# Performance work log

Measured on AMD Instinct MI355X. Metric: run time of the kernel, lower is better.

The kernel has to match this reference:

```python
import jax, jax.numpy as jnp
import numpy as np

B = 2048
LATENT = 32
FRAME = 256
COND = 1
HIDDEN = 256
FUT = 1
E = 8
GATE_H = 64
IN_SIZE = LATENT + FRAME * COND      # 288
INTER = LATENT + HIDDEN              # 288 (must equal IN_SIZE, see forward)
OUT_SIZE = FUT * FRAME               # 256


def setup_inputs() -> dict:
    key = jax.random.key(0)
    ks = jax.random.split(key, 16)

    def kaiming(k, shape, fan_in):
        bound = np.sqrt(6.0 / fan_in).astype(np.float32)
        return jax.random.uniform(k, shape, jnp.float32, -bound, bound)

    z = jax.random.normal(ks[0], (B, IN_SIZE), jnp.float32)
    # gate MLP: Linear(IN_SIZE,64) -> ELU -> Linear(64,64) -> ELU -> Linear(64,E)
    g0_w = kaiming(ks[1], (IN_SIZE, GATE_H), IN_SIZE)
    g0_b = jnp.zeros((GATE_H,), jnp.float32)
    g1_w = kaiming(ks[2], (GATE_H, GATE_H), GATE_H)
    g1_b = jnp.zeros((GATE_H,), jnp.float32)
    g2_w = kaiming(ks[3], (GATE_H, E), GATE_H)
    g2_b = jnp.zeros((E,), jnp.float32)
    # expert layers (kaiming_uniform over [E, in, out]; bias filled with 0.01)
    w0 = kaiming(ks[4], (E, IN_SIZE, HIDDEN), IN_SIZE)
    b0 = jnp.full((E, HIDDEN), 0.01, jnp.float32)
    w1 = kaiming(ks[5], (E, INTER, HIDDEN), INTER)
    b1 = jnp.full((E, HIDDEN), 0.01, jnp.float32)
    w2 = kaiming(ks[6], (E, INTER, OUT_SIZE), INTER)
    b2 = jnp.full((E, OUT_SIZE), 0.01, jnp.float32)
    return dict(z=z, g0_w=g0_w, g0_b=g0_b, g1_w=g1_w, g1_b=g1_b,
                g2_w=g2_w, g2_b=g2_b, w0=w0, b0=b0, w1=w1, b1=b1, w2=w2, b2=b2)


def reference(z, g0_w, g0_b, g1_w, g1_b, g2_w, g2_b, w0, b0, w1, b1, w2, b2):
    # gating network -> softmax coefficients [B, E]
    h = jax.nn.elu(z @ g0_w + g0_b)
    h = jax.nn.elu(h @ g1_w + g1_b)
    coefficients = jax.nn.softmax(h @ g2_w + g2_b, axis=1)

    layers = [(w0, b0, True), (w1, b1, True), (w2, b2, False)]
    layer_out = None
    for weight, bias, has_act in layers:
        # materialize per-sample mixed weights (matches torch.matmul(coef, flat_weight).view(...))
        mixed_weight = jnp.einsum('be,eio->bio', coefficients, weight)  # [B, in, out]
        mixed_bias = coefficients @ bias                                 # [B, out]
        # baddbmm with z as [B,1,in]: per-sample vec-mat product
        out = jnp.einsum('bi,bio->bo', z, mixed_weight) + mixed_bias
        layer_out = jax.nn.elu(out) if has_act else out
    return layer_out
```

## Files before the change

kernel.cpp:

```cpp
#include <hip/hip_runtime.h>
#include <hip/hip_bf16.h>

#define B_TOTAL 2048
#define IN_SZ   288
#define GH      64
#define E_NUM   8
#define OUT_N   256
#define NKT     9

#define W2F_BLKS 72
#define ZF_BLKS  32
#define GWF_FRAGS 46

typedef __attribute__((ext_vector_type(8))) short bf16x8;
typedef __attribute__((ext_vector_type(4))) float f32x4;

__device__ __forceinline__ float elu_f(float x) {
    return x > 0.0f ? x : (expf(x) - 1.0f);
}
__device__ __forceinline__ ushort f2bf(float f) {
    __hip_bfloat16 h = __float2bfloat16(f);
    return *reinterpret_cast<ushort*>(&h);
}

__global__ __launch_bounds__(256) void prep_kernel(
    const float* __restrict__ w2, const float* __restrict__ z,
    const float* __restrict__ g0_w, const float* __restrict__ g1_w,
    const float* __restrict__ g2_w,
    ushort* __restrict__ w2f, ushort* __restrict__ zf, ushort* __restrict__ gwf)
{
    __shared__ float ts[32][260];
    const int t = threadIdx.x;
    const int wid = t >> 6, l = t & 63;
    const int fr = l & 15, fg = l >> 4;

    if (blockIdx.x < W2F_BLKS) {
        const int e  = blockIdx.x / NKT;
        const int kt = blockIdx.x - e * NKT;
        const float* src = w2 + ((size_t)e * IN_SZ + kt * 32) * OUT_N;
        #pragma unroll
        for (int q = t; q < 2048; q += 256) {
            int r = q >> 6, c4 = q & 63;
            *(float4*)&ts[r][c4 * 4] = *(const float4*)(src + (size_t)r * OUT_N + c4 * 4);
        }
        __syncthreads();
        #pragma unroll
        for (int it = 0; it < 4; ++it) {
            int q = t + it * 256;
            int nt = q >> 6, ll = q & 63;
            int qfr = ll & 15, qfg = ll >> 4;
            ushort4 u0, u1;
            u0.x = f2bf(ts[qfg * 8 + 0][nt * 16 + qfr]);
            u0.y = f2bf(ts[qfg * 8 + 1][nt * 16 + qfr]);
            u0.z = f2bf(ts[qfg * 8 + 2][nt * 16 + qfr]);
            u0.w = f2bf(ts[qfg * 8 + 3][nt * 16 + qfr]);
            u1.x = f2bf(ts[qfg * 8 + 4][nt * 16 + qfr]);
            u1.y = f2bf(ts[qfg * 8 + 5][nt * 16 + qfr]);
            u1.z = f2bf(ts[qfg * 8 + 6][nt * 16 + qfr]);
            u1.w = f2bf(ts[qfg * 8 + 7][nt * 16 + qfr]);
            size_t off = ((size_t)((e * 16 + nt) * NKT + kt)) * 512 + ll * 8;
            *(ushort4*)&w2f[off]     = u0;
            *(ushort4*)&w2f[off + 4] = u1;
        }
        return;
    }

    if (blockIdx.x < W2F_BLKS + ZF_BLKS) {
        const int mt = (blockIdx.x - W2F_BLKS) * 4 + wid;
        const int m0 = mt * 16;
        const float* zr = z + (size_t)(m0 + fr) * IN_SZ + fg * 8;
        #pragma unroll
        for (int kt = 0; kt < NKT; ++kt) {
            float4 v0 = *(const float4*)(zr + kt * 32);
            float4 v1 = *(const float4*)(zr + kt * 32 + 4);
            ushort4 u0, u1;
            u0.x = f2bf(v0.x); u0.y = f2bf(v0.y); u0.z = f2bf(v0.z); u0.w = f2bf(v0.w);
            u1.x = f2bf(v1.x); u1.y = f2bf(v1.y); u1.z = f2bf(v1.z); u1.w = f2bf(v1.w);
            size_t off = ((size_t)(mt * NKT + kt)) * 512 + l * 8;
            *(ushort4*)&zf[off]     = u0;
            *(ushort4*)&zf[off + 4] = u1;
        }
        return;
    }

    for (int fid = wid; fid < GWF_FRAGS; fid += 4) {
        float vals[8];
        if (fid < 36) {
            int nt = fid / NKT, kt = fid - nt * NKT;
            #pragma unroll
            for (int j = 0; j < 8; ++j) {
                int k = kt * 32 + fg * 8 + j;
                vals[j] = g0_w[k * GH + nt * 16 + fr];
            }
        } else if (fid < 44) {
            int q = fid - 36, nt = q >> 1, kk = q & 1;
            #pragma unroll
            for (int j = 0; j < 8; ++j) {
                int k = kk * 32 + fg * 8 + j;
                vals[j] = g1_w[k * GH + nt * 16 + fr];
            }
        } else {
            int kk = fid - 44;
            #pragma unroll
            for (int j = 0; j < 8; ++j) {
                int k = kk * 32 + fg * 8 + j;
                vals[j] = (fr < E_NUM) ? g2_w[k * E_NUM + fr] : 0.0f;
            }
        }
        ushort4 u0, u1;
        u0.x = f2bf(vals[0]); u0.y = f2bf(vals[1]); u0.z = f2bf(vals[2]); u0.w = f2bf(vals[3]);
        u1.x = f2bf(vals[4]); u1.y = f2bf(vals[5]); u1.z = f2bf(vals[6]); u1.w = f2bf(vals[7]);
        size_t off = (size_t)fid * 512 + l * 8;
        *(ushort4*)&gwf[off]     = u0;
        *(ushort4*)&gwf[off + 4] = u1;
    }
}

__global__ __launch_bounds__(256) void gate_kernel(
    const ushort* __restrict__ zf, const ushort* __restrict__ gwf,
    const float* __restrict__ g0_b, const float* __restrict__ g1_b,
    const float* __restrict__ g2_b,
    float* __restrict__ coefT)
{
    __shared__ ushort hscr_all[4][16][72];
    __shared__ float  lgs[64][8];

    const int t = threadIdx.x, wid = t >> 6, l = t & 63;
    const int fr = l & 15, fg = l >> 4, fk = fg * 8;
    const int r0 = blockIdx.x * 64;
    const int mt = blockIdx.x * 4 + wid;
    ushort (*hscr)[72] = hscr_all[wid];

    bf16x8 A[9];
    #pragma unroll
    for (int kt = 0; kt < NKT; ++kt)
        A[kt] = *(const bf16x8*)(zf + ((size_t)(mt * NKT + kt)) * 512 + l * 8);

    #pragma unroll
    for (int nt = 0; nt < 4; ++nt) {
        f32x4 g = {0.f, 0.f, 0.f, 0.f};
        #pragma unroll
        for (int kt = 0; kt < NKT; ++kt) {
            bf16x8 b = *(const bf16x8*)(gwf + ((size_t)(nt * NKT + kt)) * 512 + l * 8);
            g = __builtin_amdgcn_mfma_f32_16x16x32_bf16(A[kt], b, g, 0, 0, 0);
        }
        float bias = g0_b[nt * 16 + fr];
        #pragma unroll
        for (int j = 0; j < 4; ++j)
            hscr[fg * 4 + j][nt * 16 + fr] = f2bf(elu_f(g[j] + bias));
    }

    {
        bf16x8 hA[2];
        #pragma unroll
        for (int kk = 0; kk < 2; ++kk)
            hA[kk] = *(const bf16x8*)&hscr[fr][kk * 32 + fk];
        #pragma unroll
        for (int nt = 0; nt < 4; ++nt) {
            f32x4 g = {0.f, 0.f, 0.f, 0.f};
            #pragma unroll
            for (int kk = 0; kk < 2; ++kk) {
                bf16x8 b = *(const bf16x8*)(gwf + ((size_t)(36 + nt * 2 + kk)) * 512 + l * 8);
                g = __builtin_amdgcn_mfma_f32_16x16x32_bf16(hA[kk], b, g, 0, 0, 0);
            }
            float bias = g1_b[nt * 16 + fr];
            #pragma unroll
            for (int j = 0; j < 4; ++j)
                hscr[fg * 4 + j][nt * 16 + fr] = f2bf(elu_f(g[j] + bias));
        }
    }

    {
        bf16x8 hA[2];
        #pragma unroll
        for (int kk = 0; kk < 2; ++kk)
            hA[kk] = *(const bf16x8*)&hscr[fr][kk * 32 + fk];
        f32x4 g = {0.f, 0.f, 0.f, 0.f};
        #pragma unroll
        for (int kk = 0; kk < 2; ++kk) {
            bf16x8 b = *(const bf16x8*)(gwf + ((size_t)(44 + kk)) * 512 + l * 8);
            g = __builtin_amdgcn_mfma_f32_16x16x32_bf16(hA[kk], b, g, 0, 0, 0);
        }
        if (fr < E_NUM) {
            float bias = g2_b[fr];
            #pragma unroll
            for (int j = 0; j < 4; ++j)
                lgs[wid * 16 + fg * 4 + j][fr] = g[j] + bias;
        }
    }
    __syncthreads();

    if (t < 64) {
        float m = lgs[t][0];
        #pragma unroll
        for (int k = 1; k < E_NUM; ++k) m = fmaxf(m, lgs[t][k]);
        float s = 0.f;
        float ex[E_NUM];
        #pragma unroll
        for (int k = 0; k < E_NUM; ++k) { ex[k] = expf(lgs[t][k] - m); s += ex[k]; }
        float inv = 1.0f / s;
        #pragma unroll
        for (int k = 0; k < E_NUM; ++k)
            coefT[(size_t)k * B_TOTAL + r0 + t] = ex[k] * inv;
    }
}

__global__ __launch_bounds__(64) void gemm_kernel(
    const ushort* __restrict__ zf, const ushort* __restrict__ w2f,
    const float* __restrict__ coefT, const float* __restrict__ b2,
    float* __restrict__ out)
{
    const int l = threadIdx.x, fr = l & 15, fg = l >> 4;
    const int mt = blockIdx.x, m0 = mt * 16;
    const int nt = blockIdx.y, n0 = nt * 16;

    bf16x8 A[9];
    #pragma unroll
    for (int kt = 0; kt < NKT; ++kt)
        A[kt] = *(const bf16x8*)(zf + ((size_t)(mt * NKT + kt)) * 512 + l * 8);

    const ushort* Bp = w2f + (size_t)nt * NKT * 512 + l * 8;

    f32x4 acc = {0.f, 0.f, 0.f, 0.f};
    bf16x8 B[9];
    #pragma unroll
    for (int kt = 0; kt < NKT; ++kt)
        B[kt] = *(const bf16x8*)(Bp + (size_t)kt * 512);

    #pragma unroll
    for (int e = 0; e < E_NUM; ++e) {
        bf16x8 Bn[9];
        if (e < E_NUM - 1) {
            #pragma unroll
            for (int kt = 0; kt < NKT; ++kt)
                Bn[kt] = *(const bf16x8*)(Bp + ((size_t)(e + 1) * 16 * NKT + kt) * 512);
        }
        f32x4 p0 = {0.f, 0.f, 0.f, 0.f};
        f32x4 p1 = {0.f, 0.f, 0.f, 0.f};
        p0 = __builtin_amdgcn_mfma_f32_16x16x32_bf16(A[0], B[0], p0, 0, 0, 0);
        p1 = __builtin_amdgcn_mfma_f32_16x16x32_bf16(A[1], B[1], p1, 0, 0, 0);
        p0 = __builtin_amdgcn_mfma_f32_16x16x32_bf16(A[2], B[2], p0, 0, 0, 0);
        p1 = __builtin_amdgcn_mfma_f32_16x16x32_bf16(A[3], B[3], p1, 0, 0, 0);
        p0 = __builtin_amdgcn_mfma_f32_16x16x32_bf16(A[4], B[4], p0, 0, 0, 0);
        p1 = __builtin_amdgcn_mfma_f32_16x16x32_bf16(A[5], B[5], p1, 0, 0, 0);
        p0 = __builtin_amdgcn_mfma_f32_16x16x32_bf16(A[6], B[6], p0, 0, 0, 0);
        p1 = __builtin_amdgcn_mfma_f32_16x16x32_bf16(A[7], B[7], p1, 0, 0, 0);
        p0 = __builtin_amdgcn_mfma_f32_16x16x32_bf16(A[8], B[8], p0, 0, 0, 0);

        float4 cv = *(const float4*)(coefT + (size_t)e * B_TOTAL + m0 + fg * 4);
        float bv  = b2[e * OUT_N + n0 + fr];
        float ca[4] = {cv.x, cv.y, cv.z, cv.w};
        #pragma unroll
        for (int j = 0; j < 4; ++j)
            acc[j] = fmaf(ca[j], p0[j] + p1[j] + bv, acc[j]);

        #pragma unroll
        for (int kt = 0; kt < NKT; ++kt) B[kt] = Bn[kt];
    }

    #pragma unroll
    for (int j = 0; j < 4; ++j)
        out[(size_t)(m0 + fg * 4 + j) * OUT_N + n0 + fr] = acc[j];
}

__global__ __launch_bounds__(64) void gate_fb_kernel(
    const float* __restrict__ z,
    const float* __restrict__ g0_w, const float* __restrict__ g0_b,
    const float* __restrict__ g1_w, const float* __restrict__ g1_b,
    const float* __restrict__ g2_w, const float* __restrict__ g2_b,
    float* __restrict__ coef)
{
    __shared__ float z_s[IN_SZ];
    __shared__ float h0_s[GH];
    __shared__ float h1_s[GH];
    const int b = blockIdx.x;
    const int t = threadIdx.x;
    const float* zr = z + (size_t)b * IN_SZ;
    for (int i = t; i < IN_SZ; i += 64) z_s[i] = zr[i];
    __syncthreads();
    float a0 = g0_b[t];
    for (int i = 0; i < IN_SZ; ++i) a0 = fmaf(z_s[i], g0_w[i * GH + t], a0);
    h0_s[t] = elu_f(a0);
    __syncthreads();
    float a1 = g1_b[t];
    for (int k = 0; k < GH; ++k) a1 = fmaf(h0_s[k], g1_w[k * GH + t], a1);
    h1_s[t] = elu_f(a1);
    __syncthreads();
    if (t < E_NUM) {
        float lg = g2_b[t];
        for (int k = 0; k < GH; ++k) lg = fmaf(h1_s[k], g2_w[k * E_NUM + t], lg);
        float m = lg;
        for (int d = 1; d < 8; d <<= 1) m = fmaxf(m, __shfl_xor(m, d, 8));
        float ex = expf(lg - m);
        float s = ex;
        for (int d = 1; d < 8; d <<= 1) s += __shfl_xor(s, d, 8);
        coef[b * E_NUM + t] = ex / s;
    }
}

__global__ __launch_bounds__(256) void direct_kernel(
    const float* __restrict__ z, const float* __restrict__ w2,
    const float* __restrict__ b2, const float* __restrict__ coef,
    float* __restrict__ out)
{
    __shared__ float z_s[8][IN_SZ];
    __shared__ float c_s[8][E_NUM];
    const int b0 = blockIdx.x * 8;
    const int t  = threadIdx.x;
    for (int idx = t; idx < 8 * IN_SZ; idx += 256)
        ((float*)z_s)[idx] = z[(size_t)b0 * IN_SZ + idx];
    if (t < 64) c_s[t >> 3][t & 7] = coef[b0 * E_NUM + t];
    __syncthreads();
    float outv[8];
    #pragma unroll
    for (int r = 0; r < 8; ++r) outv[r] = 0.0f;
    for (int e = 0; e < E_NUM; ++e) {
        const float* w = w2 + (size_t)e * IN_SZ * OUT_N + t;
        float tmp[8];
        #pragma unroll
        for (int r = 0; r < 8; ++r) tmp[r] = 0.0f;
        #pragma unroll 4
        for (int i = 0; i < IN_SZ; ++i) {
            float wv = w[i * OUT_N];
            #pragma unroll
            for (int r = 0; r < 8; ++r) tmp[r] += z_s[r][i] * wv;
        }
        float bv = b2[e * OUT_N + t];
        #pragma unroll
        for (int r = 0; r < 8; ++r) outv[r] += c_s[r][e] * (tmp[r] + bv);
    }
    #pragma unroll
    for (int r = 0; r < 8; ++r) out[(size_t)(b0 + r) * OUT_N + t] = outv[r];
}

extern "C" void kernel_launch(void* const* d_in, const int* in_sizes, int n_in,
                              void* d_out, int out_size, void* d_ws, size_t ws_size,
                              hipStream_t stream) {
    const float* z    = (const float*)d_in[0];
    const float* g0_w = (const float*)d_in[1];
    const float* g0_b = (const float*)d_in[2];
    const float* g1_w = (const float*)d_in[3];
    const float* g1_b = (const float*)d_in[4];
    const float* g2_w = (const float*)d_in[5];
    const float* g2_b = (const float*)d_in[6];
    const float* w2   = (const float*)d_in[11];
    const float* b2   = (const float*)d_in[12];
    float* out = (float*)d_out;

    const size_t w2f_b   = (size_t)E_NUM * 16 * NKT * 1024;
    const size_t zf_b    = (size_t)128 * NKT * 1024;
    const size_t gwf_b   = (size_t)GWF_FRAGS * 1024;
    const size_t coefT_b = (size_t)E_NUM * B_TOTAL * sizeof(float);

    char* p = (char*)d_ws;
    ushort* w2f   = (ushort*)p;            p += w2f_b;
    ushort* zf    = (ushort*)p;            p += zf_b;
    ushort* gwf   = (ushort*)p;            p += gwf_b;
    float*  coefT = (float*)p;

    if (ws_size >= w2f_b + zf_b + gwf_b + coefT_b) {
        prep_kernel<<<W2F_BLKS + ZF_BLKS + 1, 256, 0, stream>>>(
            w2, z, g0_w, g1_w, g2_w, w2f, zf, gwf);
        gate_kernel<<<32, 256, 0, stream>>>(zf, gwf, g0_b, g1_b, g2_b, coefT);
        gemm_kernel<<<dim3(B_TOTAL / 16, OUT_N / 16), 64, 0, stream>>>(
            zf, w2f, coefT, b2, out);
    } else {
        float* coef = (float*)d_ws;
        gate_fb_kernel<<<B_TOTAL, 64, 0, stream>>>(z, g0_w, g0_b, g1_w, g1_b,
                                                   g2_w, g2_b, coef);
        direct_kernel<<<B_TOTAL / 8, 256, 0, stream>>>(z, w2, b2, coef, out);
    }
}
```

Measured before the change: 24.20 us.

## Fuse gate network into prep kernel and tile GEMM over two row tiles

The gating MLP is folded into the prep kernel: the z-conversion blocks now also run the gate, reading gate weights straight from fp32 and converting them to bf16 in registers instead of going through a separate gate kernel and a pre-packed weight buffer. This removes one kernel launch and the gwf round trip, at the cost of redundant gate-weight loads and conversions in every block, plus extra block-wide barriers. The GEMM kernel now computes two 16-row tiles per block, reusing each loaded expert weight fragment for both tiles and halving the grid, which raises register pressure.

```diff
diff --git a/kernel.cpp b/kernel.cpp
--- a/kernel.cpp
+++ b/kernel.cpp
@@ -9,8 +9,7 @@
 #define NKT     9
 
 #define W2F_BLKS 72
-#define ZF_BLKS  32
-#define GWF_FRAGS 46
+#define ZG_BLKS  32
 
 typedef __attribute__((ext_vector_type(8))) short bf16x8;
 typedef __attribute__((ext_vector_type(4))) float f32x4;
@@ -25,16 +24,18 @@
 
 __global__ __launch_bounds__(256) void prep_kernel(
     const float* __restrict__ w2, const float* __restrict__ z,
-    const float* __restrict__ g0_w, const float* __restrict__ g1_w,
-    const float* __restrict__ g2_w,
-    ushort* __restrict__ w2f, ushort* __restrict__ zf, ushort* __restrict__ gwf)
+    const float* __restrict__ g0_w, const float* __restrict__ g0_b,
+    const float* __restrict__ g1_w, const float* __restrict__ g1_b,
+    const float* __restrict__ g2_w, const float* __restrict__ g2_b,
+    ushort* __restrict__ w2f, ushort* __restrict__ zf, float* __restrict__ coefT)
 {
-    __shared__ float ts[32][260];
+    __shared__ char smem[33536];
     const int t = threadIdx.x;
     const int wid = t >> 6, l = t & 63;
     const int fr = l & 15, fg = l >> 4;
 
     if (blockIdx.x < W2F_BLKS) {
+        float (*ts)[260] = (float(*)[260])smem;
         const int e  = blockIdx.x / NKT;
         const int kt = blockIdx.x - e * NKT;
         const float* src = w2 + ((size_t)e * IN_SZ + kt * 32) * OUT_N;
@@ -65,83 +66,39 @@
         return;
     }
 
-    if (blockIdx.x < W2F_BLKS + ZF_BLKS) {
-        const int mt = (blockIdx.x - W2F_BLKS) * 4 + wid;
-        const int m0 = mt * 16;
-        const float* zr = z + (size_t)(m0 + fr) * IN_SZ + fg * 8;
-        #pragma unroll
-        for (int kt = 0; kt < NKT; ++kt) {
-            float4 v0 = *(const float4*)(zr + kt * 32);
-            float4 v1 = *(const float4*)(zr + kt * 32 + 4);
-            ushort4 u0, u1;
-            u0.x = f2bf(v0.x); u0.y = f2bf(v0.y); u0.z = f2bf(v0.z); u0.w = f2bf(v0.w);
-            u1.x = f2bf(v1.x); u1.y = f2bf(v1.y); u1.z = f2bf(v1.z); u1.w = f2bf(v1.w);
-            size_t off = ((size_t)(mt * NKT + kt)) * 512 + l * 8;
-            *(ushort4*)&zf[off]     = u0;
-            *(ushort4*)&zf[off + 4] = u1;
-        }
-        return;
-    }
-
-    for (int fid = wid; fid < GWF_FRAGS; fid += 4) {
-        float vals[8];
-        if (fid < 36) {
-            int nt = fid / NKT, kt = fid - nt * NKT;
-            #pragma unroll
-            for (int j = 0; j < 8; ++j) {
-                int k = kt * 32 + fg * 8 + j;
-                vals[j] = g0_w[k * GH + nt * 16 + fr];
-            }
-        } else if (fid < 44) {
-            int q = fid - 36, nt = q >> 1, kk = q & 1;
-            #pragma unroll
-            for (int j = 0; j < 8; ++j) {
-                int k = kk * 32 + fg * 8 + j;
-                vals[j] = g1_w[k * GH + nt * 16 + fr];
-            }
-        } else {
-            int kk = fid - 44;
-            #pragma unroll
-            for (int j = 0; j < 8; ++j) {
-                int k = kk * 32 + fg * 8 + j;
-                vals[j] = (fr < E_NUM) ? g2_w[k * E_NUM + fr] : 0.0f;
-            }
-        }
-        ushort4 u0, u1;
-        u0.x = f2bf(vals[0]); u0.y = f2bf(vals[1]); u0.z = f2bf(vals[2]); u0.w = f2bf(vals[3]);
-        u1.x = f2bf(vals[4]); u1.y = f2bf(vals[5]); u1.z = f2bf(vals[6]); u1.w = f2bf(vals[7]);
-        size_t off = (size_t)fid * 512 + l * 8;
-        *(ushort4*)&gwf[off]     = u0;
-        *(ushort4*)&gwf[off + 4] = u1;
-    }
-}
-
-__global__ __launch_bounds__(256) void gate_kernel(
-    const ushort* __restrict__ zf, const ushort* __restrict__ gwf,
-    const float* __restrict__ g0_b, const float* __restrict__ g1_b,
-    const float* __restrict__ g2_b,
-    float* __restrict__ coefT)
-{
-    __shared__ ushort hscr_all[4][16][72];
-    __shared__ float  lgs[64][8];
-
-    const int t = threadIdx.x, wid = t >> 6, l = t & 63;
-    const int fr = l & 15, fg = l >> 4, fk = fg * 8;
-    const int r0 = blockIdx.x * 64;
-    const int mt = blockIdx.x * 4 + wid;
-    ushort (*hscr)[72] = hscr_all[wid];
+    ushort (*hscr)[72] = (ushort(*)[72])(smem + wid * 2304);
+    float  (*lgs)[8]   = (float(*)[8])(smem + 4 * 2304 + wid * 512);
+
+    const int mt = (blockIdx.x - W2F_BLKS) * 4 + wid;
+    const int m0 = mt * 16;
 
     bf16x8 A[9];
-    #pragma unroll
-    for (int kt = 0; kt < NKT; ++kt)
-        A[kt] = *(const bf16x8*)(zf + ((size_t)(mt * NKT + kt)) * 512 + l * 8);
+    const float* zr = z + (size_t)(m0 + fr) * IN_SZ + fg * 8;
+    #pragma unroll
+    for (int kt = 0; kt < NKT; ++kt) {
+        float4 v0 = *(const float4*)(zr + kt * 32);
+        float4 v1 = *(const float4*)(zr + kt * 32 + 4);
+        bf16x8 a;
+        a[0] = (short)f2bf(v0.x); a[1] = (short)f2bf(v0.y);
+        a[2] = (short)f2bf(v0.z); a[3] = (short)f2bf(v0.w);
+        a[4] = (short)f2bf(v1.x); a[5] = (short)f2bf(v1.y);
+        a[6] = (short)f2bf(v1.z); a[7] = (short)f2bf(v1.w);
+        A[kt] = a;
+        *(bf16x8*)(zf + ((size_t)(mt * NKT + kt)) * 512 + l * 8) = a;
+    }
 
     #pragma unroll
     for (int nt = 0; nt < 4; ++nt) {
         f32x4 g = {0.f, 0.f, 0.f, 0.f};
         #pragma unroll
         for (int kt = 0; kt < NKT; ++kt) {
-            bf16x8 b = *(const bf16x8*)(gwf + ((size_t)(nt * NKT + kt)) * 512 + l * 8);
+            float vals[8];
+            #pragma unroll
+            for (int j = 0; j < 8; ++j)
+                vals[j] = g0_w[(kt * 32 + fg * 8 + j) * GH + nt * 16 + fr];
+            bf16x8 b;
+            #pragma unroll
+            for (int j = 0; j < 8; ++j) b[j] = (short)f2bf(vals[j]);
             g = __builtin_amdgcn_mfma_f32_16x16x32_bf16(A[kt], b, g, 0, 0, 0);
         }
         float bias = g0_b[nt * 16 + fr];
@@ -149,59 +106,79 @@
         for (int j = 0; j < 4; ++j)
             hscr[fg * 4 + j][nt * 16 + fr] = f2bf(elu_f(g[j] + bias));
     }
+    __syncthreads();
 
     {
         bf16x8 hA[2];
         #pragma unroll
         for (int kk = 0; kk < 2; ++kk)
-            hA[kk] = *(const bf16x8*)&hscr[fr][kk * 32 + fk];
+            hA[kk] = *(const bf16x8*)&hscr[fr][kk * 32 + fg * 8];
+        f32x4 gacc[4];
         #pragma unroll
         for (int nt = 0; nt < 4; ++nt) {
             f32x4 g = {0.f, 0.f, 0.f, 0.f};
             #pragma unroll
             for (int kk = 0; kk < 2; ++kk) {
-                bf16x8 b = *(const bf16x8*)(gwf + ((size_t)(36 + nt * 2 + kk)) * 512 + l * 8);
+                float vals[8];
+                #pragma unroll
+                for (int j = 0; j < 8; ++j)
+                    vals[j] = g1_w[(kk * 32 + fg * 8 + j) * GH + nt * 16 + fr];
+                bf16x8 b;
+                #pragma unroll
+                for (int j = 0; j < 8; ++j) b[j] = (short)f2bf(vals[j]);
                 g = __builtin_amdgcn_mfma_f32_16x16x32_bf16(hA[kk], b, g, 0, 0, 0);
             }
+            gacc[nt] = g;
+        }
+        __syncthreads();
+        #pragma unroll
+        for (int nt = 0; nt < 4; ++nt) {
             float bias = g1_b[nt * 16 + fr];
             #pragma unroll
             for (int j = 0; j < 4; ++j)
-                hscr[fg * 4 + j][nt * 16 + fr] = f2bf(elu_f(g[j] + bias));
-        }
-    }
+                hscr[fg * 4 + j][nt * 16 + fr] = f2bf(elu_f(gacc[nt][j] + bias));
+        }
+    }
+    __syncthreads();
 
     {
         bf16x8 hA[2];
         #pragma unroll
         for (int kk = 0; kk < 2; ++kk)
-            hA[kk] = *(const bf16x8*)&hscr[fr][kk * 32 + fk];
+            hA[kk] = *(const bf16x8*)&hscr[fr][kk * 32 + fg * 8];
         f32x4 g = {0.f, 0.f, 0.f, 0.f};
         #pragma unroll
         for (int kk = 0; kk < 2; ++kk) {
-            bf16x8 b = *(const bf16x8*)(gwf + ((size_t)(44 + kk)) * 512 + l * 8);
+            float vals[8];
+            #pragma unroll
+            for (int j = 0; j < 8; ++j)
+                vals[j] = (fr < E_NUM) ? g2_w[(kk * 32 + fg * 8 + j) * E_NUM + fr] : 0.0f;
+            bf16x8 b;
+            #pragma unroll
+            for (int j = 0; j < 8; ++j) b[j] = (short)f2bf(vals[j]);
             g = __builtin_amdgcn_mfma_f32_16x16x32_bf16(hA[kk], b, g, 0, 0, 0);
         }
         if (fr < E_NUM) {
             float bias = g2_b[fr];
             #pragma unroll
             for (int j = 0; j < 4; ++j)
-                lgs[wid * 16 + fg * 4 + j][fr] = g[j] + bias;
-        }
-    }
-    __syncthreads();
-
-    if (t < 64) {
-        float m = lgs[t][0];
-        #pragma unroll
-        for (int k = 1; k < E_NUM; ++k) m = fmaxf(m, lgs[t][k]);
+                lgs[fg * 4 + j][fr] = g[j] + bias;
+        }
+    }
+    __syncthreads();
+
+    if (l < 16) {
+        float m = lgs[l][0];
+        #pragma unroll
+        for (int k = 1; k < E_NUM; ++k) m = fmaxf(m, lgs[l][k]);
         float s = 0.f;
         float ex[E_NUM];
         #pragma unroll
-        for (int k = 0; k < E_NUM; ++k) { ex[k] = expf(lgs[t][k] - m); s += ex[k]; }
+        for (int k = 0; k < E_NUM; ++k) { ex[k] = expf(lgs[l][k] - m); s += ex[k]; }
         float inv = 1.0f / s;
         #pragma unroll
         for (int k = 0; k < E_NUM; ++k)
-            coefT[(size_t)k * B_TOTAL + r0 + t] = ex[k] * inv;
+            coefT[(size_t)k * B_TOTAL + m0 + l] = ex[k] * inv;
     }
 }
 
@@ -211,17 +188,20 @@
     float* __restrict__ out)
 {
     const int l = threadIdx.x, fr = l & 15, fg = l >> 4;
-    const int mt = blockIdx.x, m0 = mt * 16;
+    const int mt0 = blockIdx.x * 2, m0 = mt0 * 16;
     const int nt = blockIdx.y, n0 = nt * 16;
 
-    bf16x8 A[9];
-    #pragma unroll
-    for (int kt = 0; kt < NKT; ++kt)
-        A[kt] = *(const bf16x8*)(zf + ((size_t)(mt * NKT + kt)) * 512 + l * 8);
+    bf16x8 A0[9], A1[9];
+    #pragma unroll
+    for (int kt = 0; kt < NKT; ++kt) {
+        A0[kt] = *(const bf16x8*)(zf + ((size_t)(mt0 * NKT + kt)) * 512 + l * 8);
+        A1[kt] = *(const bf16x8*)(zf + ((size_t)((mt0 + 1) * NKT + kt)) * 512 + l * 8);
+    }
 
     const ushort* Bp = w2f + (size_t)nt * NKT * 512 + l * 8;
 
-    f32x4 acc = {0.f, 0.f, 0.f, 0.f};
+    f32x4 acc0 = {0.f, 0.f, 0.f, 0.f};
+    f32x4 acc1 = {0.f, 0.f, 0.f, 0.f};
     bf16x8 B[9];
     #pragma unroll
     for (int kt = 0; kt < NKT; ++kt)
@@ -233,34 +213,39 @@
         if (e < E_NUM - 1) {
             #pragma unroll
             for (int kt = 0; kt < NKT; ++kt)
-                Bn[kt] = *(const bf16x8*)(Bp + ((size_t)(e + 1) * 16 * NKT + kt) * 512);
-        }
-        f32x4 p0 = {0.f, 0.f, 0.f, 0.f};
-        f32x4 p1 = {0.f, 0.f, 0.f, 0.f};
-        p0 = __builtin_amdgcn_mfma_f32_16x16x32_bf16(A[0], B[0], p0, 0, 0, 0);
-        p1 = __builtin_amdgcn_mfma_f32_16x16x32_bf16(A[1], B[1], p1, 0, 0, 0);
-        p0 = __builtin_amdgcn_mfma_f32_16x16x32_bf16(A[2], B[2], p0, 0, 0, 0);
-        p1 = __builtin_amdgcn_mfma_f32_16x16x32_bf16(A[3], B[3], p1, 0, 0, 0);
-        p0 = __builtin_amdgcn_mfma_f32_16x16x32_bf16(A[4], B[4], p0, 0, 0, 0);
-        p1 = __builtin_amdgcn_mfma_f32_16x16x32_bf16(A[5], B[5], p1, 0, 0, 0);
-        p0 = __builtin_amdgcn_mfma_f32_16x16x32_bf16(A[6], B[6], p0, 0, 0, 0);
-        p1 = __builtin_amdgcn_mfma_f32_16x16x32_bf16(A[7], B[7], p1, 0, 0, 0);
-        p0 = __builtin_amdgcn_mfma_f32_16x16x32_bf16(A[8], B[8], p0, 0, 0, 0);
-
-        float4 cv = *(const float4*)(coefT + (size_t)e * B_TOTAL + m0 + fg * 4);
+                Bn[kt] = *(const bf16x8*)(Bp + ((size_t)((e + 1) * 16 * NKT) + kt) * 512);
+        }
+        f32x4 p00 = {0.f, 0.f, 0.f, 0.f}, p01 = {0.f, 0.f, 0.f, 0.f};
+        f32x4 p10 = {0.f, 0.f, 0.f, 0.f}, p11 = {0.f, 0.f, 0.f, 0.f};
+        #pragma unroll
+        for (int kt = 0; kt < 4; ++kt) {
+            p00 = __builtin_amdgcn_mfma_f32_16x16x32_bf16(A0[kt], B[kt], p00, 0, 0, 0);
+            p10 = __builtin_amdgcn_mfma_f32_16x16x32_bf16(A1[kt], B[kt], p10, 0, 0, 0);
+            p01 = __builtin_amdgcn_mfma_f32_16x16x32_bf16(A0[kt + 4], B[kt + 4], p01, 0, 0, 0);
+            p11 = __builtin_amdgcn_mfma_f32_16x16x32_bf16(A1[kt + 4], B[kt + 4], p11, 0, 0, 0);
+        }
+        p00 = __builtin_amdgcn_mfma_f32_16x16x32_bf16(A0[8], B[8], p00, 0, 0, 0);
+        p10 = __builtin_amdgcn_mfma_f32_16x16x32_bf16(A1[8], B[8], p10, 0, 0, 0);
+
+        float4 c0 = *(const float4*)(coefT + (size_t)e * B_TOTAL + m0 + fg * 4);
+        float4 c1 = *(const float4*)(coefT + (size_t)e * B_TOTAL + m0 + 16 + fg * 4);
         float bv  = b2[e * OUT_N + n0 + fr];
-        float ca[4] = {cv.x, cv.y, cv.z, cv.w};
-        #pragma unroll
-        for (int j = 0; j < 4; ++j)
-            acc[j] = fmaf(ca[j], p0[j] + p1[j] + bv, acc[j]);
-
+        float c0a[4] = {c0.x, c0.y, c0.z, c0.w};
+        float c1a[4] = {c1.x, c1.y, c1.z, c1.w};
+        #pragma unroll
+        for (int j = 0; j < 4; ++j) {
+            acc0[j] = fmaf(c0a[j], p00[j] + p01[j] + bv, acc0[j]);
+            acc1[j] = fmaf(c1a[j], p10[j] + p11[j] + bv, acc1[j]);
+        }
         #pragma unroll
         for (int kt = 0; kt < NKT; ++kt) B[kt] = Bn[kt];
     }
 
     #pragma unroll
-    for (int j = 0; j < 4; ++j)
-        out[(size_t)(m0 + fg * 4 + j) * OUT_N + n0 + fr] = acc[j];
+    for (int j = 0; j < 4; ++j) {
+        out[(size_t)(m0 + fg * 4 + j) * OUT_N + n0 + fr]      = acc0[j];
+        out[(size_t)(m0 + 16 + fg * 4 + j) * OUT_N + n0 + fr] = acc1[j];
+    }
 }
 
 __global__ __launch_bounds__(64) void gate_fb_kernel(
@@ -349,20 +334,17 @@
 
     const size_t w2f_b   = (size_t)E_NUM * 16 * NKT * 1024;
     const size_t zf_b    = (size_t)128 * NKT * 1024;
-    const size_t gwf_b   = (size_t)GWF_FRAGS * 1024;
     const size_t coefT_b = (size_t)E_NUM * B_TOTAL * sizeof(float);
 
     char* p = (char*)d_ws;
     ushort* w2f   = (ushort*)p;            p += w2f_b;
     ushort* zf    = (ushort*)p;            p += zf_b;
-    ushort* gwf   = (ushort*)p;            p += gwf_b;
     float*  coefT = (float*)p;
 
-    if (ws_size >= w2f_b + zf_b + gwf_b + coefT_b) {
-        prep_kernel<<<W2F_BLKS + ZF_BLKS + 1, 256, 0, stream>>>(
-            w2, z, g0_w, g1_w, g2_w, w2f, zf, gwf);
-        gate_kernel<<<32, 256, 0, stream>>>(zf, gwf, g0_b, g1_b, g2_b, coefT);
-        gemm_kernel<<<dim3(B_TOTAL / 16, OUT_N / 16), 64, 0, stream>>>(
+    if (ws_size >= w2f_b + zf_b + coefT_b) {
+        prep_kernel<<<W2F_BLKS + ZG_BLKS, 256, 0, stream>>>(
+            w2, z, g0_w, g0_b, g1_w, g1_b, g2_w, g2_b, w2f, zf, coefT);
+        gemm_kernel<<<dim3(B_TOTAL / 32, OUT_N / 16), 64, 0, stream>>>(
             zf, w2f, coefT, b2, out);
     } else {
         float* coef = (float*)d_ws;
```

Measured after the change: 31.52 us. 1.3x slower.

## Split gate into per-tile blocks and split expert loop across two waves

Applied to the files above, without the earlier changes.

The gate kernel now launches 128 single-wave blocks, one 16-row tile each, instead of 32 four-wave blocks, which spreads the small gating work over more CUs. The expert GEMM kernel now uses two waves per output tile, each handling four experts, and combines the partial accumulators through shared memory before one wave writes the result. This aims to shorten the serial per-expert MFMA chain and raise parallelism, at the cost of an extra barrier, a shared-memory exchange, and loading the A fragments twice per block.

```diff
diff --git a/kernel.cpp b/kernel.cpp
--- a/kernel.cpp
+++ b/kernel.cpp
@@ -116,20 +116,19 @@
     }
 }
 
-__global__ __launch_bounds__(256) void gate_kernel(
+__global__ __launch_bounds__(64) void gate_kernel(
     const ushort* __restrict__ zf, const ushort* __restrict__ gwf,
     const float* __restrict__ g0_b, const float* __restrict__ g1_b,
     const float* __restrict__ g2_b,
     float* __restrict__ coefT)
 {
-    __shared__ ushort hscr_all[4][16][72];
-    __shared__ float  lgs[64][8];
-
-    const int t = threadIdx.x, wid = t >> 6, l = t & 63;
+    __shared__ ushort hscr[16][72];
+    __shared__ float  lgs[16][8];
+
+    const int l = threadIdx.x;
     const int fr = l & 15, fg = l >> 4, fk = fg * 8;
-    const int r0 = blockIdx.x * 64;
-    const int mt = blockIdx.x * 4 + wid;
-    ushort (*hscr)[72] = hscr_all[wid];
+    const int mt = blockIdx.x;
+    const int m0 = mt * 16;
 
     bf16x8 A[9];
     #pragma unroll
@@ -149,12 +148,14 @@
         for (int j = 0; j < 4; ++j)
             hscr[fg * 4 + j][nt * 16 + fr] = f2bf(elu_f(g[j] + bias));
     }
+    __syncthreads();
 
     {
         bf16x8 hA[2];
         #pragma unroll
         for (int kk = 0; kk < 2; ++kk)
             hA[kk] = *(const bf16x8*)&hscr[fr][kk * 32 + fk];
+        f32x4 gacc[4];
         #pragma unroll
         for (int nt = 0; nt < 4; ++nt) {
             f32x4 g = {0.f, 0.f, 0.f, 0.f};
@@ -163,12 +164,18 @@
                 bf16x8 b = *(const bf16x8*)(gwf + ((size_t)(36 + nt * 2 + kk)) * 512 + l * 8);
                 g = __builtin_amdgcn_mfma_f32_16x16x32_bf16(hA[kk], b, g, 0, 0, 0);
             }
+            gacc[nt] = g;
+        }
+        __syncthreads();
+        #pragma unroll
+        for (int nt = 0; nt < 4; ++nt) {
             float bias = g1_b[nt * 16 + fr];
             #pragma unroll
             for (int j = 0; j < 4; ++j)
-                hscr[fg * 4 + j][nt * 16 + fr] = f2bf(elu_f(g[j] + bias));
-        }
-    }
+                hscr[fg * 4 + j][nt * 16 + fr] = f2bf(elu_f(gacc[nt][j] + bias));
+        }
+    }
+    __syncthreads();
 
     {
         bf16x8 hA[2];
@@ -185,32 +192,34 @@
             float bias = g2_b[fr];
             #pragma unroll
             for (int j = 0; j < 4; ++j)
-                lgs[wid * 16 + fg * 4 + j][fr] = g[j] + bias;
-        }
-    }
-    __syncthreads();
-
-    if (t < 64) {
-        float m = lgs[t][0];
-        #pragma unroll
-        for (int k = 1; k < E_NUM; ++k) m = fmaxf(m, lgs[t][k]);
+                lgs[fg * 4 + j][fr] = g[j] + bias;
+        }
+    }
+    __syncthreads();
+
+    if (l < 16) {
+        float m = lgs[l][0];
+        #pragma unroll
+        for (int k = 1; k < E_NUM; ++k) m = fmaxf(m, lgs[l][k]);
         float s = 0.f;
         float ex[E_NUM];
         #pragma unroll
-        for (int k = 0; k < E_NUM; ++k) { ex[k] = expf(lgs[t][k] - m); s += ex[k]; }
+        for (int k = 0; k < E_NUM; ++k) { ex[k] = expf(lgs[l][k] - m); s += ex[k]; }
         float inv = 1.0f / s;
         #pragma unroll
         for (int k = 0; k < E_NUM; ++k)
-            coefT[(size_t)k * B_TOTAL + r0 + t] = ex[k] * inv;
-    }
-}
-
-__global__ __launch_bounds__(64) void gemm_kernel(
+            coefT[(size_t)k * B_TOTAL + m0 + l] = ex[k] * inv;
+    }
+}
+
+__global__ __launch_bounds__(128) void gemm_kernel(
     const ushort* __restrict__ zf, const ushort* __restrict__ w2f,
     const float* __restrict__ coefT, const float* __restrict__ b2,
     float* __restrict__ out)
 {
-    const int l = threadIdx.x, fr = l & 15, fg = l >> 4;
+    __shared__ float xfer[64][4];
+    const int t = threadIdx.x, wv = t >> 6, l = t & 63;
+    const int fr = l & 15, fg = l >> 4;
     const int mt = blockIdx.x, m0 = mt * 16;
     const int nt = blockIdx.y, n0 = nt * 16;
 
@@ -220,20 +229,22 @@
         A[kt] = *(const bf16x8*)(zf + ((size_t)(mt * NKT + kt)) * 512 + l * 8);
 
     const ushort* Bp = w2f + (size_t)nt * NKT * 512 + l * 8;
+    const int e0 = wv * 4;
 
     f32x4 acc = {0.f, 0.f, 0.f, 0.f};
     bf16x8 B[9];
     #pragma unroll
     for (int kt = 0; kt < NKT; ++kt)
-        B[kt] = *(const bf16x8*)(Bp + (size_t)kt * 512);
-
-    #pragma unroll
-    for (int e = 0; e < E_NUM; ++e) {
+        B[kt] = *(const bf16x8*)(Bp + ((size_t)(e0 * 16 * NKT) + kt) * 512);
+
+    #pragma unroll
+    for (int ee = 0; ee < 4; ++ee) {
+        const int e = e0 + ee;
         bf16x8 Bn[9];
-        if (e < E_NUM - 1) {
+        if (ee < 3) {
             #pragma unroll
             for (int kt = 0; kt < NKT; ++kt)
-                Bn[kt] = *(const bf16x8*)(Bp + ((size_t)(e + 1) * 16 * NKT + kt) * 512);
+                Bn[kt] = *(const bf16x8*)(Bp + ((size_t)((e + 1) * 16 * NKT) + kt) * 512);
         }
         f32x4 p0 = {0.f, 0.f, 0.f, 0.f};
         f32x4 p1 = {0.f, 0.f, 0.f, 0.f};
@@ -258,9 +269,16 @@
         for (int kt = 0; kt < NKT; ++kt) B[kt] = Bn[kt];
     }
 
-    #pragma unroll
-    for (int j = 0; j < 4; ++j)
-        out[(size_t)(m0 + fg * 4 + j) * OUT_N + n0 + fr] = acc[j];
+    if (wv == 1) {
+        #pragma unroll
+        for (int j = 0; j < 4; ++j) xfer[l][j] = acc[j];
+    }
+    __syncthreads();
+    if (wv == 0) {
+        #pragma unroll
+        for (int j = 0; j < 4; ++j)
+            out[(size_t)(m0 + fg * 4 + j) * OUT_N + n0 + fr] = acc[j] + xfer[l][j];
+    }
 }
 
 __global__ __launch_bounds__(64) void gate_fb_kernel(
@@ -361,8 +379,8 @@
     if (ws_size >= w2f_b + zf_b + gwf_b + coefT_b) {
         prep_kernel<<<W2F_BLKS + ZF_BLKS + 1, 256, 0, stream>>>(
             w2, z, g0_w, g1_w, g2_w, w2f, zf, gwf);
-        gate_kernel<<<32, 256, 0, stream>>>(zf, gwf, g0_b, g1_b, g2_b, coefT);
-        gemm_kernel<<<dim3(B_TOTAL / 16, OUT_N / 16), 64, 0, stream>>>(
+        gate_kernel<<<128, 64, 0, stream>>>(zf, gwf, g0_b, g1_b, g2_b, coefT);
+        gemm_kernel<<<dim3(B_TOTAL / 16, OUT_N / 16), 128, 0, stream>>>(
             zf, w2f, coefT, b2, out);
     } else {
         float* coef = (float*)d_ws;
```

Result: slower. 25.61 us (+5.8%).

## Fuse gating MLP and softmax into the expert GEMM kernel

Applied to the files above, without the earlier changes.

Merges the gate kernel into the GEMM kernel. Each 128-thread block recomputes the gate MLP and softmax for its two 16-row tiles and keeps the coefficients in shared memory instead of writing coefT to global. This removes one kernel launch and the global round trip for the coefficients. The cost is redundant gate computation across all 16 column tiles and extra block barriers. The gate-weight prep is also spread over four blocks instead of one.

```diff
diff --git a/kernel.cpp b/kernel.cpp
--- a/kernel.cpp
+++ b/kernel.cpp
@@ -10,6 +10,7 @@
 
 #define W2F_BLKS 72
 #define ZF_BLKS  32
+#define GWF_BLKS 4
 #define GWF_FRAGS 46
 
 typedef __attribute__((ext_vector_type(8))) short bf16x8;
@@ -83,7 +84,8 @@
         return;
     }
 
-    for (int fid = wid; fid < GWF_FRAGS; fid += 4) {
+    const int base = (blockIdx.x - W2F_BLKS - ZF_BLKS) * 4 + wid;
+    for (int fid = base; fid < GWF_FRAGS; fid += 16) {
         float vals[8];
         if (fid < 36) {
             int nt = fid / NKT, kt = fid - nt * NKT;
@@ -116,20 +118,21 @@
     }
 }
 
-__global__ __launch_bounds__(256) void gate_kernel(
-    const ushort* __restrict__ zf, const ushort* __restrict__ gwf,
+__global__ __launch_bounds__(128) void fused_kernel(
+    const ushort* __restrict__ zf, const ushort* __restrict__ w2f,
+    const ushort* __restrict__ gwf,
     const float* __restrict__ g0_b, const float* __restrict__ g1_b,
-    const float* __restrict__ g2_b,
-    float* __restrict__ coefT)
+    const float* __restrict__ g2_b, const float* __restrict__ b2,
+    float* __restrict__ out)
 {
-    __shared__ ushort hscr_all[4][16][72];
-    __shared__ float  lgs[64][8];
-
-    const int t = threadIdx.x, wid = t >> 6, l = t & 63;
+    __shared__ ushort hscr[2][16][72];
+    __shared__ float  lgs[2][16][8];
+    __shared__ float  cfsT[2][E_NUM][16];
+
+    const int t = threadIdx.x, wv = t >> 6, l = t & 63;
     const int fr = l & 15, fg = l >> 4, fk = fg * 8;
-    const int r0 = blockIdx.x * 64;
-    const int mt = blockIdx.x * 4 + wid;
-    ushort (*hscr)[72] = hscr_all[wid];
+    const int mt = blockIdx.x * 2 + wv, m0 = mt * 16;
+    const int nt = blockIdx.y, n0 = nt * 16;
 
     bf16x8 A[9];
     #pragma unroll
@@ -137,44 +140,52 @@
         A[kt] = *(const bf16x8*)(zf + ((size_t)(mt * NKT + kt)) * 512 + l * 8);
 
     #pragma unroll
-    for (int nt = 0; nt < 4; ++nt) {
+    for (int ng = 0; ng < 4; ++ng) {
         f32x4 g = {0.f, 0.f, 0.f, 0.f};
         #pragma unroll
         for (int kt = 0; kt < NKT; ++kt) {
-            bf16x8 b = *(const bf16x8*)(gwf + ((size_t)(nt * NKT + kt)) * 512 + l * 8);
+            bf16x8 b = *(const bf16x8*)(gwf + ((size_t)(ng * NKT + kt)) * 512 + l * 8);
             g = __builtin_amdgcn_mfma_f32_16x16x32_bf16(A[kt], b, g, 0, 0, 0);
         }
-        float bias = g0_b[nt * 16 + fr];
+        float bias = g0_b[ng * 16 + fr];
         #pragma unroll
         for (int j = 0; j < 4; ++j)
-            hscr[fg * 4 + j][nt * 16 + fr] = f2bf(elu_f(g[j] + bias));
-    }
+            hscr[wv][fg * 4 + j][ng * 16 + fr] = f2bf(elu_f(g[j] + bias));
+    }
+    __syncthreads();
 
     {
         bf16x8 hA[2];
         #pragma unroll
         for (int kk = 0; kk < 2; ++kk)
-            hA[kk] = *(const bf16x8*)&hscr[fr][kk * 32 + fk];
-        #pragma unroll
-        for (int nt = 0; nt < 4; ++nt) {
+            hA[kk] = *(const bf16x8*)&hscr[wv][fr][kk * 32 + fk];
+        f32x4 gacc[4];
+        #pragma unroll
+        for (int ng = 0; ng < 4; ++ng) {
             f32x4 g = {0.f, 0.f, 0.f, 0.f};
             #pragma unroll
             for (int kk = 0; kk < 2; ++kk) {
-                bf16x8 b = *(const bf16x8*)(gwf + ((size_t)(36 + nt * 2 + kk)) * 512 + l * 8);
+                bf16x8 b = *(const bf16x8*)(gwf + ((size_t)(36 + ng * 2 + kk)) * 512 + l * 8);
                 g = __builtin_amdgcn_mfma_f32_16x16x32_bf16(hA[kk], b, g, 0, 0, 0);
             }
-            float bias = g1_b[nt * 16 + fr];
+            gacc[ng] = g;
+        }
+        __syncthreads();
+        #pragma unroll
+        for (int ng = 0; ng < 4; ++ng) {
+            float bias = g1_b[ng * 16 + fr];
             #pragma unroll
             for (int j = 0; j < 4; ++j)
-                hscr[fg * 4 + j][nt * 16 + fr] = f2bf(elu_f(g[j] + bias));
-        }
-    }
+                hscr[wv][fg * 4 + j][ng * 16 + fr] = f2bf(elu_f(gacc[ng][j] + bias));
+        }
+    }
+    __syncthreads();
 
     {
         bf16x8 hA[2];
         #pragma unroll
         for (int kk = 0; kk < 2; ++kk)
-            hA[kk] = *(const bf16x8*)&hscr[fr][kk * 32 + fk];
+            hA[kk] = *(const bf16x8*)&hscr[wv][fr][kk * 32 + fk];
         f32x4 g = {0.f, 0.f, 0.f, 0.f};
         #pragma unroll
         for (int kk = 0; kk < 2; ++kk) {
@@ -185,39 +196,24 @@
             float bias = g2_b[fr];
             #pragma unroll
             for (int j = 0; j < 4; ++j)
-                lgs[wid * 16 + fg * 4 + j][fr] = g[j] + bias;
-        }
-    }
-    __syncthreads();
-
-    if (t < 64) {
-        float m = lgs[t][0];
-        #pragma unroll
-        for (int k = 1; k < E_NUM; ++k) m = fmaxf(m, lgs[t][k]);
+                lgs[wv][fg * 4 + j][fr] = g[j] + bias;
+        }
+    }
+    __syncthreads();
+
+    if (l < 16) {
+        float m = lgs[wv][l][0];
+        #pragma unroll
+        for (int k = 1; k < E_NUM; ++k) m = fmaxf(m, lgs[wv][l][k]);
         float s = 0.f;
         float ex[E_NUM];
         #pragma unroll
-        for (int k = 0; k < E_NUM; ++k) { ex[k] = expf(lgs[t][k] - m); s += ex[k]; }
+        for (int k = 0; k < E_NUM; ++k) { ex[k] = expf(lgs[wv][l][k] - m); s += ex[k]; }
         float inv = 1.0f / s;
         #pragma unroll
-        for (int k = 0; k < E_NUM; ++k)
-            coefT[(size_t)k * B_TOTAL + r0 + t] = ex[k] * inv;
-    }
-}
-
-__global__ __launch_bounds__(64) void gemm_kernel(
-    const ushort* __restrict__ zf, const ushort* __restrict__ w2f,
-    const float* __restrict__ coefT, const float* __restrict__ b2,
-    float* __restrict__ out)
-{
-    const int l = threadIdx.x, fr = l & 15, fg = l >> 4;
-    const int mt = blockIdx.x, m0 = mt * 16;
-    const int nt = blockIdx.y, n0 = nt * 16;
-
-    bf16x8 A[9];
-    #pragma unroll
-    for (int kt = 0; kt < NKT; ++kt)
-        A[kt] = *(const bf16x8*)(zf + ((size_t)(mt * NKT + kt)) * 512 + l * 8);
+        for (int k = 0; k < E_NUM; ++k) cfsT[wv][k][l] = ex[k] * inv;
+    }
+    __syncthreads();
 
     const ushort* Bp = w2f + (size_t)nt * NKT * 512 + l * 8;
 
@@ -233,7 +229,7 @@
         if (e < E_NUM - 1) {
             #pragma unroll
             for (int kt = 0; kt < NKT; ++kt)
-                Bn[kt] = *(const bf16x8*)(Bp + ((size_t)(e + 1) * 16 * NKT + kt) * 512);
+                Bn[kt] = *(const bf16x8*)(Bp + ((size_t)((e + 1) * 16 * NKT) + kt) * 512);
         }
         f32x4 p0 = {0.f, 0.f, 0.f, 0.f};
         f32x4 p1 = {0.f, 0.f, 0.f, 0.f};
@@ -247,7 +243,7 @@
         p1 = __builtin_amdgcn_mfma_f32_16x16x32_bf16(A[7], B[7], p1, 0, 0, 0);
         p0 = __builtin_amdgcn_mfma_f32_16x16x32_bf16(A[8], B[8], p0, 0, 0, 0);
 
-        float4 cv = *(const float4*)(coefT + (size_t)e * B_TOTAL + m0 + fg * 4);
+        float4 cv = *(const float4*)&cfsT[wv][e][fg * 4];
         float bv  = b2[e * OUT_N + n0 + fr];
         float ca[4] = {cv.x, cv.y, cv.z, cv.w};
         #pragma unroll
@@ -347,23 +343,20 @@
     const float* b2   = (const float*)d_in[12];
     float* out = (float*)d_out;
 
-    const size_t w2f_b   = (size_t)E_NUM * 16 * NKT * 1024;
-    const size_t zf_b    = (size_t)128 * NKT * 1024;
-    const size_t gwf_b   = (size_t)GWF_FRAGS * 1024;
-    const size_t coefT_b = (size_t)E_NUM * B_TOTAL * sizeof(float);
+    const size_t w2f_b = (size_t)E_NUM * 16 * NKT * 1024;
+    const size_t zf_b  = (size_t)128 * NKT * 1024;
+    const size_t gwf_b = (size_t)GWF_FRAGS * 1024;
 
     char* p = (char*)d_ws;
-    ushort* w2f   = (ushort*)p;            p += w2f_b;
-    ushort* zf    = (ushort*)p;            p += zf_b;
-    ushort* gwf   = (ushort*)p;            p += gwf_b;
-    float*  coefT = (float*)p;
-
-    if (ws_size >= w2f_b + zf_b + gwf_b + coefT_b) {
-        prep_kernel<<<W2F_BLKS + ZF_BLKS + 1, 256, 0, stream>>>(
+    ushort* w2f = (ushort*)p;            p += w2f_b;
+    ushort* zf  = (ushort*)p;            p += zf_b;
+    ushort* gwf = (ushort*)p;
+
+    if (ws_size >= w2f_b + zf_b + gwf_b) {
+        prep_kernel<<<W2F_BLKS + ZF_BLKS + GWF_BLKS, 256, 0, stream>>>(
             w2, z, g0_w, g1_w, g2_w, w2f, zf, gwf);
-        gate_kernel<<<32, 256, 0, stream>>>(zf, gwf, g0_b, g1_b, g2_b, coefT);
-        gemm_kernel<<<dim3(B_TOTAL / 16, OUT_N / 16), 64, 0, stream>>>(
-            zf, w2f, coefT, b2, out);
+        fused_kernel<<<dim3(B_TOTAL / 32, OUT_N / 16), 128, 0, stream>>>(
+            zf, w2f, gwf, g0_b, g1_b, g2_b, b2, out);
     } else {
         float* coef = (float*)d_ws;
         gate_fb_kernel<<<B_TOTAL, 64, 0, stream>>>(z, g0_w, g0_b, g1_w, g1_b,
```

Measured after the change: 22.63 us. 1.07x faster.
